# Performance work log

Hardware: AMD Instinct MI355X
Metric: run time of the kernel (lower is better)

Reference implementation:

```python
import jax, jax.numpy as jnp
import numpy as np

EPS = 1e-5
LORA_DIM = 64
LORA_SCALE = LORA_DIM ** (-0.5)
GRAD_SCALE = 0.5  # infeat_grad_scale (bp_to_unet=True path)


def _ln(x, g=None, b=None):
    mu = jnp.mean(x, axis=-1, keepdims=True)
    var = jnp.mean((x - mu) ** 2, axis=-1, keepdims=True)
    y = (x - mu) * jax.lax.rsqrt(var + EPS)
    if g is not None:
        y = y * g + b
    return y


def _grad_scale(t, s=GRAD_SCALE):
    # identity in forward, scales gradient by s in backward
    return t * s + jax.lax.stop_gradient(t) * (1.0 - s)


def setup_inputs() -> dict:
    key = jax.random.key(0)
    ks = jax.random.split(key, 8)
    B, C, H, W = 32, 1280, 32, 32
    TD, LD = 768, LORA_DIM
    inp = {}
    inp["layer_infeat"] = jax.random.normal(ks[0], (B, C, H, W), jnp.float32)
    inp["layer_inquery"] = jax.random.normal(ks[1], (B, H * W, C), jnp.float32)
    inp["token_q_emb"] = jax.random.normal(ks[2], (TD,), jnp.float32)
    # learned params
    inp["to_q_w"] = jax.random.normal(ks[3], (C, TD), jnp.float32) * (TD ** -0.5)
    inp["ln_x_g"] = jnp.ones((C,), jnp.float32)
    inp["ln_x_b"] = jnp.zeros((C,), jnp.float32)
    inp["ln_k_g"] = jnp.ones((C,), jnp.float32)
    inp["ln_k_b"] = jnp.zeros((C,), jnp.float32)
    inp["ln_q_g"] = jnp.ones((TD,), jnp.float32)
    inp["ln_q_b"] = jnp.zeros((TD,), jnp.float32)
    inp["lora_q_w"] = jax.random.normal(ks[4], (LD, C), jnp.float32) * (C ** -0.5)
    inp["lora_k_w"] = jax.random.normal(ks[5], (LD, C), jnp.float32) * (C ** -0.5)
    inp["mask"] = jax.random.randint(ks[6], (B, 1, H, W), 0, 2).astype(jnp.float32)
    return inp


def reference(layer_infeat, layer_inquery, token_q_emb, to_q_w,
              ln_x_g, ln_x_b, ln_k_g, ln_k_b, ln_q_g, ln_q_b,
              lora_q_w, lora_k_w, mask):
    B, C, H, W = layer_infeat.shape
    # flatten(2).permute(0,2,1): [B,C,H,W] -> [B, HW, C]
    x = _grad_scale(layer_infeat).reshape(B, C, H * W).transpose(0, 2, 1)
    k_in = _grad_scale(layer_inquery)
    # q = to_q(ln_q(token_q_emb[None])) -> [1, C], broadcast to [B, 1, C]
    q = _ln(token_q_emb[None, :], ln_q_g, ln_q_b) @ to_q_w.T
    q = jnp.broadcast_to(q[None], (B, 1, C))
    k = _ln(k_in, ln_k_g, ln_k_b)   # [B, HW, C]
    v = _ln(x, ln_x_g, ln_x_b)      # [B, HW, C]
    # LoRA score path (use_lora=True since lora_dim>0)
    lora_q = _ln(q) @ lora_q_w.T    # [B, 1, LD]
    lora_k = _ln(k) @ lora_k_w.T    # [B, HW, LD]
    sim = jnp.einsum('bid,bjd->bij', lora_q, lora_k) * LORA_SCALE  # [B,1,HW]
    # mask: nearest interpolation to (H,W) is identity (same size); flatten
    m = mask.reshape(B, 1, H * W) > 0
    sim = jnp.where(m, sim, -jnp.finfo(sim.dtype).max)
    attn = jax.nn.softmax(sim, axis=-1)
    fg = jnp.einsum('bij,bjd->bid', attn, v)            # [B, 1, C]
    bg = jnp.mean(v, axis=1, keepdims=True) - fg        # [B, 1, C]
    out = jnp.concatenate([fg, bg], axis=-1)            # [B, 1, 2C]
    return out[:, 0, :]                                  # [B, 2C]
```

## Files before the change

### kernel.cpp

```cpp
#include <hip/hip_runtime.h>
#include <math.h>

#define B_   32
#define CD   1280
#define HW_  1024
#define TD_  768
#define LD_  64
#define EPSF 1e-5f
#define LORA_SCALE_F 0.125f

__device__ __forceinline__ float wredSum(float a) {
#pragma unroll
  for (int o = 32; o; o >>= 1) a += __shfl_xor(a, o, 64);
  return a;
}
__device__ __forceinline__ void wred2(float& a, float& b) {
#pragma unroll
  for (int o = 32; o; o >>= 1) { a += __shfl_xor(a, o, 64); b += __shfl_xor(b, o, 64); }
}
__device__ __forceinline__ void wred3(float& a, float& b, float& c) {
#pragma unroll
  for (int o = 32; o; o >>= 1) {
    a += __shfl_xor(a, o, 64); b += __shfl_xor(b, o, 64); c += __shfl_xor(c, o, 64);
  }
}
template<int N>
__device__ __forceinline__ void wredN(float* v) {
#pragma unroll
  for (int o = 32; o; o >>= 1) {
#pragma unroll
    for (int k = 0; k < N; k++) v[k] += __shfl_xor(v[k], o, 64);
  }
}
__device__ __forceinline__ void blockSum2(float& a, float& b, float2* red) {
  int t = threadIdx.x;
  red[t] = make_float2(a, b); __syncthreads();
#pragma unroll
  for (int s = 128; s > 0; s >>= 1) {
    if (t < s) { red[t].x += red[t + s].x; red[t].y += red[t + s].y; }
    __syncthreads();
  }
  a = red[0].x; b = red[0].y; __syncthreads();
}

__global__ __launch_bounds__(256) void kA12(const float* __restrict__ tq,
                                            const float* __restrict__ lng,
                                            const float* __restrict__ lnb,
                                            const float* __restrict__ to_q_w,
                                            float* __restrict__ q_out) {
  __shared__ float lnq[TD_];
  __shared__ float2 red[256];
  int t = threadIdx.x;
  float s = 0.f, ss = 0.f, vals[3];
#pragma unroll
  for (int k = 0; k < 3; k++) { float v = tq[t + 256 * k]; vals[k] = v; s += v; ss += v * v; }
  blockSum2(s, ss, red);
  float mu = s * (1.f / TD_);
  float r = rsqrtf(ss * (1.f / TD_) - mu * mu + EPSF);
#pragma unroll
  for (int k = 0; k < 3; k++) { int i = t + 256 * k; lnq[i] = (vals[k] - mu) * r * lng[i] + lnb[i]; }
  __syncthreads();
  int c = blockIdx.x * 4 + (t >> 6);
  int lane = t & 63;
  const float4* w4 = (const float4*)(to_q_w + (size_t)c * TD_);
  const float4* l4 = (const float4*)lnq;
  float dot = 0.f;
#pragma unroll
  for (int i = 0; i < 3; i++) {
    int f = i * 64 + lane;
    float4 w = w4[f], l = l4[f];
    dot += w.x * l.x + w.y * l.y + w.z * l.z + w.w * l.w;
  }
  dot = wredSum(dot);
  if (lane == 0) q_out[c] = dot;
}

__global__ __launch_bounds__(256) void kA3456(const float* __restrict__ q_in,
                                              const float* __restrict__ lora_q_w,
                                              const float* __restrict__ lora_k_w,
                                              float* __restrict__ w_eff) {
  __shared__ float qn[CD];
  __shared__ float lq[LD_];
  __shared__ float redS[8];
  int t = threadIdx.x;
  int wid = t >> 6, lane = t & 63;
  float s = 0.f, ss = 0.f, vals[5];
#pragma unroll
  for (int k = 0; k < 5; k++) { float v = q_in[t + 256 * k]; vals[k] = v; s += v; ss += v * v; }
  wred2(s, ss);
  if (lane == 0) { redS[wid * 2] = s; redS[wid * 2 + 1] = ss; }
  __syncthreads();
  s = redS[0] + redS[2] + redS[4] + redS[6];
  ss = redS[1] + redS[3] + redS[5] + redS[7];
  float mu = s * (1.f / CD);
  float r = rsqrtf(ss * (1.f / CD) - mu * mu + EPSF);
#pragma unroll
  for (int k = 0; k < 5; k++) { int i = t + 256 * k; qn[i] = (vals[k] - mu) * r; }
  __syncthreads();
  {
    int gg = t >> 2, sub = t & 3;
    const float4* w4 = (const float4*)(lora_q_w + (size_t)gg * CD);
    const float4* q4 = (const float4*)qn;
    float dot = 0.f;
#pragma unroll 8
    for (int i = 0; i < 80; i++) {
      int f = i * 4 + sub;
      float4 w = w4[f], qq = q4[f];
      dot += w.x * qq.x + w.y * qq.y + w.z * qq.z + w.w * qq.w;
    }
    dot += __shfl_xor(dot, 1, 64);
    dot += __shfl_xor(dot, 2, 64);
    if (sub == 0) lq[gg] = dot;
  }
  __syncthreads();
  int c = blockIdx.x * 256 + t;
  float acc = 0.f;
#pragma unroll 8
  for (int d = 0; d < LD_; d++) acc += lq[d] * lora_k_w[(size_t)d * CD + c];
  w_eff[c] = acc;
}

__global__ __launch_bounds__(256, 4) void kBD1(const float* __restrict__ kin,
                                               const float* __restrict__ g,
                                               const float* __restrict__ bb,
                                               const float* __restrict__ w_eff,
                                               float* __restrict__ sim,
                                               const float* __restrict__ infeat,
                                               float* __restrict__ mu_out,
                                               float* __restrict__ r_out) {
  __shared__ float smem[5152];
  int t = threadIdx.x;
  int m5 = blockIdx.x % 5, d5 = blockIdx.x / 5;
  int wid = t >> 6, lane = t & 63;
  if (m5 != 4) {
    int kbid = d5 * 4 + m5;
    float* cg  = smem;
    float* cg2 = smem + 1280;
    float* cgb = smem + 2560;
    float* cwg = smem + 3840;
    float* red = smem + 5120;
    float p[8] = {0.f,0.f,0.f,0.f,0.f,0.f,0.f,0.f};
    for (int kk = t; kk < 320; kk += 256) {
      float4 g4 = ((const float4*)g)[kk];
      float4 b4 = ((const float4*)bb)[kk];
      float4 w4 = ((const float4*)w_eff)[kk];
      float4 q4  = make_float4(g4.x*g4.x, g4.y*g4.y, g4.z*g4.z, g4.w*g4.w);
      float4 gb4 = make_float4(g4.x*b4.x, g4.y*b4.y, g4.z*b4.z, g4.w*b4.w);
      float4 wg4 = make_float4(w4.x*g4.x, w4.y*g4.y, w4.z*g4.z, w4.w*g4.w);
      ((float4*)cg)[kk]  = g4;
      ((float4*)cg2)[kk] = q4;
      ((float4*)cgb)[kk] = gb4;
      ((float4*)cwg)[kk] = wg4;
      p[0] += g4.x + g4.y + g4.z + g4.w;
      p[1] += b4.x + b4.y + b4.z + b4.w;
      p[2] += q4.x + q4.y + q4.z + q4.w;
      p[3] += gb4.x + gb4.y + gb4.z + gb4.w;
      p[4] += b4.x*b4.x + b4.y*b4.y + b4.z*b4.z + b4.w*b4.w;
      p[5] += wg4.x + wg4.y + wg4.z + wg4.w;
      p[6] += w4.x*b4.x + w4.y*b4.y + w4.z*b4.z + w4.w*b4.w;
      p[7] += w4.x + w4.y + w4.z + w4.w;
    }
    wredN<8>(p);
    if (lane == 0) {
#pragma unroll
      for (int j = 0; j < 8; j++) red[wid * 8 + j] = p[j];
    }
    __syncthreads();
    float G0 = red[0] + red[8]  + red[16] + red[24];
    float B0 = red[1] + red[9]  + red[17] + red[25];
    float G2 = red[2] + red[10] + red[18] + red[26];
    float GB = red[3] + red[11] + red[19] + red[27];
    float B2 = red[4] + red[12] + red[20] + red[28];
    float WG = red[5] + red[13] + red[21] + red[29];
    float WB = red[6] + red[14] + red[22] + red[30];
    float W0 = red[7] + red[15] + red[23] + red[31];
    const float invC = 1.f / CD;
    const float4* cg4  = (const float4*)cg;
    const float4* cg24 = (const float4*)cg2;
    const float4* cgb4 = (const float4*)cgb;
    const float4* cwg4 = (const float4*)cwg;

    int gw = kbid * 4 + wid;
#pragma unroll
    for (int m = 0; m < 2; m++) {
      int rowA = gw + 16384 * m;
      int rowB = rowA + 8192;
      const float4* xA = (const float4*)(kin + (size_t)rowA * CD);
      const float4* xB = (const float4*)(kin + (size_t)rowB * CD);
      float v[14];
#pragma unroll
      for (int k = 0; k < 14; k++) v[k] = 0.f;
#pragma unroll
      for (int i = 0; i < 5; i++) {
        int f = i * 64 + lane;
        float4 xa = xA[f], xb = xB[f];
        float4 c1 = cg4[f], c2 = cg24[f], c3 = cgb4[f], c4 = cwg4[f];
#define ACC(X, Gc, G2c, GBc, WGc, o) { \
        float x_ = (X); float x2_ = x_ * x_; \
        v[(o)+0] += x_; v[(o)+1] += x2_; \
        v[(o)+2] = fmaf((Gc),  x_,  v[(o)+2]); \
        v[(o)+3] = fmaf((G2c), x_,  v[(o)+3]); \
        v[(o)+4] = fmaf((G2c), x2_, v[(o)+4]); \
        v[(o)+5] = fmaf((GBc), x_,  v[(o)+5]); \
        v[(o)+6] = fmaf((WGc), x_,  v[(o)+6]); }
        ACC(xa.x, c1.x, c2.x, c3.x, c4.x, 0)
        ACC(xa.y, c1.y, c2.y, c3.y, c4.y, 0)
        ACC(xa.z, c1.z, c2.z, c3.z, c4.z, 0)
        ACC(xa.w, c1.w, c2.w, c3.w, c4.w, 0)
        ACC(xb.x, c1.x, c2.x, c3.x, c4.x, 7)
        ACC(xb.y, c1.y, c2.y, c3.y, c4.y, 7)
        ACC(xb.z, c1.z, c2.z, c3.z, c4.z, 7)
        ACC(xb.w, c1.w, c2.w, c3.w, c4.w, 7)
#undef ACC
      }
      wredN<14>(v);
      float mu1a = v[0] * invC;
      float r1a  = rsqrtf(v[1] * invC - mu1a * mu1a + EPSF);
      float s2a  = r1a * (v[2] - mu1a * G0) + B0;
      float mu2a = s2a * invC;
      float ss2a = r1a * r1a * (v[4] - 2.f * mu1a * v[3] + mu1a * mu1a * G2)
                 + 2.f * r1a * (v[5] - mu1a * GB) + B2;
      float r2a  = rsqrtf(ss2a * invC - mu2a * mu2a + EPSF);
      float dta  = r1a * (v[6] - mu1a * WG) + WB;
      float simA = LORA_SCALE_F * r2a * (dta - mu2a * W0);
      float mu1b = v[7] * invC;
      float r1b  = rsqrtf(v[8] * invC - mu1b * mu1b + EPSF);
      float s2b  = r1b * (v[9] - mu1b * G0) + B0;
      float mu2b = s2b * invC;
      float ss2b = r1b * r1b * (v[11] - 2.f * mu1b * v[10] + mu1b * mu1b * G2)
                 + 2.f * r1b * (v[12] - mu1b * GB) + B2;
      float r2b  = rsqrtf(ss2b * invC - mu2b * mu2b + EPSF);
      float dtb  = r1b * (v[13] - mu1b * WG) + WB;
      float simB = LORA_SCALE_F * r2b * (dtb - mu2b * W0);
      if (lane == 0) { sim[rowA] = simA; sim[rowB] = simB; }
    }
  } else {
    int blk = d5;
    int tile = blk & 15, b = blk >> 4;
    int jg = t & 15;
    int slice = t >> 4;
    int j0 = tile * 64 + jg * 4;
    const float* base = infeat + (size_t)b * CD * HW_ + j0;
    float4 s = make_float4(0, 0, 0, 0), q = make_float4(0, 0, 0, 0);
    int c0 = slice * 80;
#pragma unroll 8
    for (int c = c0; c < c0 + 80; c++) {
      float4 v = *(const float4*)(base + (size_t)c * HW_);
      s.x += v.x; s.y += v.y; s.z += v.z; s.w += v.w;
      q.x += v.x * v.x; q.y += v.y * v.y; q.z += v.z * v.z; q.w += v.w * v.w;
    }
    float4* sArr = (float4*)smem;
    float4* qArr = ((float4*)smem) + 256;
    sArr[slice * 16 + jg] = s; qArr[slice * 16 + jg] = q;
    __syncthreads();
#pragma unroll
    for (int st = 8; st > 0; st >>= 1) {
      if (slice < st) {
        float4 a = sArr[slice * 16 + jg], b2 = sArr[(slice + st) * 16 + jg];
        a.x += b2.x; a.y += b2.y; a.z += b2.z; a.w += b2.w;
        sArr[slice * 16 + jg] = a;
        a = qArr[slice * 16 + jg]; b2 = qArr[(slice + st) * 16 + jg];
        a.x += b2.x; a.y += b2.y; a.z += b2.z; a.w += b2.w;
        qArr[slice * 16 + jg] = a;
      }
      __syncthreads();
    }
    if (slice == 0) {
      float4 S = sArr[jg], Q = qArr[jg], mu, r;
      mu.x = S.x * (1.f / CD); mu.y = S.y * (1.f / CD);
      mu.z = S.z * (1.f / CD); mu.w = S.w * (1.f / CD);
      r.x = rsqrtf(Q.x * (1.f / CD) - mu.x * mu.x + EPSF);
      r.y = rsqrtf(Q.y * (1.f / CD) - mu.y * mu.y + EPSF);
      r.z = rsqrtf(Q.z * (1.f / CD) - mu.z * mu.z + EPSF);
      r.w = rsqrtf(Q.w * (1.f / CD) - mu.w * mu.w + EPSF);
      int j = b * HW_ + j0;
      *(float4*)(mu_out + j) = mu;
      *(float4*)(r_out + j) = r;
    }
  }
}

__global__ __launch_bounds__(256, 4) void kD2f(const float* __restrict__ infeat,
                                               const float* __restrict__ sim,
                                               const float* __restrict__ mask,
                                               const float* __restrict__ mu,
                                               const float* __restrict__ r,
                                               const float* __restrict__ g,
                                               const float* __restrict__ bb,
                                               float* __restrict__ out) {
  __shared__ float4 w1s[HW_ / 4], w2s[HW_ / 4];
  __shared__ float red[16];
  int t = threadIdx.x;
  int b = blockIdx.x / 40, tile = blockIdx.x % 40;
  int wid = t >> 6, lane = t & 63;

  float4 sv = ((const float4*)(sim + b * HW_))[t];
  float4 mv = ((const float4*)(mask + b * HW_))[t];
  float4 muv = ((const float4*)(mu + b * HW_))[t];
  float4 rv = ((const float4*)(r + b * HW_))[t];
  const float NEG = -3.4028235e38f;
  float se0 = mv.x > 0.f ? sv.x : NEG;
  float se1 = mv.y > 0.f ? sv.y : NEG;
  float se2 = mv.z > 0.f ? sv.z : NEG;
  float se3 = mv.w > 0.f ? sv.w : NEG;
  float m = fmaxf(fmaxf(se0, se1), fmaxf(se2, se3));
#pragma unroll
  for (int o = 32; o; o >>= 1) m = fmaxf(m, __shfl_xor(m, o, 64));
  if (lane == 0) red[wid] = m;
  __syncthreads();
  float M = fmaxf(fmaxf(red[0], red[1]), fmaxf(red[2], red[3]));
  float e0 = expf(se0 - M), e1 = expf(se1 - M), e2 = expf(se2 - M), e3 = expf(se3 - M);
  float Z = e0 + e1 + e2 + e3;
  float t1 = e0 * rv.x * muv.x + e1 * rv.y * muv.y + e2 * rv.z * muv.z + e3 * rv.w * muv.w;
  float t3 = rv.x * muv.x + rv.y * muv.y + rv.z * muv.z + rv.w * muv.w;
  wred3(Z, t1, t3);
  __syncthreads();
  if (lane == 0) { red[4 + wid * 3] = Z; red[5 + wid * 3] = t1; red[6 + wid * 3] = t3; }
  __syncthreads();
  Z  = red[4] + red[7] + red[10] + red[13];
  t1 = red[5] + red[8] + red[11] + red[14];
  t3 = red[6] + red[9] + red[12] + red[15];
  float inv = 1.f / Z;
  float s1 = t1 * inv;
  float s3 = t3 * (1.f / HW_);
  w1s[t] = make_float4(e0 * rv.x * inv, e1 * rv.y * inv, e2 * rv.z * inv, e3 * rv.w * inv);
  w2s[t] = make_float4(rv.x * (1.f / HW_), rv.y * (1.f / HW_),
                       rv.z * (1.f / HW_), rv.w * (1.f / HW_));
  __syncthreads();

  int cbase = tile * 32 + wid * 8;
  const float* bbase = infeat + (size_t)b * CD * HW_;
  float v[16];
#pragma unroll
  for (int k = 0; k < 16; k++) v[k] = 0.f;
#pragma unroll
  for (int i = 0; i < 4; i++) {
    int f = i * 64 + lane;
    float4 a = w1s[f], w = w2s[f];
#pragma unroll
    for (int k = 0; k < 8; k++) {
      float4 x = ((const float4*)(bbase + (size_t)(cbase + k) * HW_))[f];
      v[2 * k]     += x.x * a.x + x.y * a.y + x.z * a.z + x.w * a.w;
      v[2 * k + 1] += x.x * w.x + x.y * w.y + x.z * w.z + x.w * w.w;
    }
  }
  wredN<16>(v);
  if (lane == 0) {
#pragma unroll
    for (int k = 0; k < 8; k++) {
      int c = cbase + k;
      float gc = g[c], bc = bb[c];
      float fg = gc * (v[2 * k] - s1) + bc;
      float vm = gc * (v[2 * k + 1] - s3) + bc;
      out[(size_t)b * (2 * CD) + c] = fg;
      out[(size_t)b * (2 * CD) + CD + c] = vm - fg;
    }
  }
}

extern "C" void kernel_launch(void* const* d_in, const int* in_sizes, int n_in,
                              void* d_out, int out_size, void* d_ws, size_t ws_size,
                              hipStream_t stream) {
  const float* infeat  = (const float*)d_in[0];
  const float* inquery = (const float*)d_in[1];
  const float* tq      = (const float*)d_in[2];
  const float* to_q_w  = (const float*)d_in[3];
  const float* ln_x_g  = (const float*)d_in[4];
  const float* ln_x_b  = (const float*)d_in[5];
  const float* ln_k_g  = (const float*)d_in[6];
  const float* ln_k_b  = (const float*)d_in[7];
  const float* ln_q_g  = (const float*)d_in[8];
  const float* ln_q_b  = (const float*)d_in[9];
  const float* lora_q_w = (const float*)d_in[10];
  const float* lora_k_w = (const float*)d_in[11];
  const float* mask    = (const float*)d_in[12];
  float* out = (float*)d_out;

  float* ws = (float*)d_ws;
  float* q_ws    = ws;
  float* weff_ws = ws + 1280;
  float* sim_ws  = ws + 2560;
  float* mu_ws   = ws + 35328;
  float* r_ws    = ws + 68096;

  kA12<<<320, 256, 0, stream>>>(tq, ln_q_g, ln_q_b, to_q_w, q_ws);
  kA3456<<<5, 256, 0, stream>>>(q_ws, lora_q_w, lora_k_w, weff_ws);
  kBD1<<<2560, 256, 0, stream>>>(inquery, ln_k_g, ln_k_b, weff_ws, sim_ws,
                                 infeat, mu_ws, r_ws);
  kD2f<<<1280, 256, 0, stream>>>(infeat, sim_ws, mask, mu_ws, r_ws,
                                 ln_x_g, ln_x_b, out);
}
```

Baseline: 416.0 us.

## Rebalance kBD1 block split, shrink shared memory, raise occupancy target

Changes the interleaving of LayerNorm-K blocks and infeat-stats blocks from 4:1 to 2:1, with smaller stats tiles (32 columns, 40-channel slices), and launches 3072 blocks. The shared-memory staging now holds g, b and w_eff instead of four precomputed products, and the accumulation uses u=g*x to form the same sums. Launch bounds rise to 8 blocks per CU. The goal is higher occupancy and better overlap of the two memory-bound streams, at the cost of a few extra multiplies per element and more register pressure under the tighter bound.

```diff
diff --git a/kernel.cpp b/kernel.cpp
--- a/kernel.cpp
+++ b/kernel.cpp
@@ -120,7 +120,7 @@
   w_eff[c] = acc;
 }
 
-__global__ __launch_bounds__(256, 4) void kBD1(const float* __restrict__ kin,
+__global__ __launch_bounds__(256, 8) void kBD1(const float* __restrict__ kin,
                                                const float* __restrict__ g,
                                                const float* __restrict__ bb,
                                                const float* __restrict__ w_eff,
@@ -128,35 +128,30 @@
                                                const float* __restrict__ infeat,
                                                float* __restrict__ mu_out,
                                                float* __restrict__ r_out) {
-  __shared__ float smem[5152];
-  int t = threadIdx.x;
-  int m5 = blockIdx.x % 5, d5 = blockIdx.x / 5;
+  __shared__ __align__(16) float smem[3872];
+  int t = threadIdx.x;
+  int m3 = blockIdx.x % 3, d3 = blockIdx.x / 3;
   int wid = t >> 6, lane = t & 63;
-  if (m5 != 4) {
-    int kbid = d5 * 4 + m5;
-    float* cg  = smem;
-    float* cg2 = smem + 1280;
-    float* cgb = smem + 2560;
-    float* cwg = smem + 3840;
-    float* red = smem + 5120;
+  if (m3 != 2) {
+    int kbid = d3 * 2 + m3;
+    float* cg = smem;
+    float* cb = smem + 1280;
+    float* cw = smem + 2560;
+    float* red = smem + 3840;
     float p[8] = {0.f,0.f,0.f,0.f,0.f,0.f,0.f,0.f};
     for (int kk = t; kk < 320; kk += 256) {
       float4 g4 = ((const float4*)g)[kk];
       float4 b4 = ((const float4*)bb)[kk];
       float4 w4 = ((const float4*)w_eff)[kk];
-      float4 q4  = make_float4(g4.x*g4.x, g4.y*g4.y, g4.z*g4.z, g4.w*g4.w);
-      float4 gb4 = make_float4(g4.x*b4.x, g4.y*b4.y, g4.z*b4.z, g4.w*b4.w);
-      float4 wg4 = make_float4(w4.x*g4.x, w4.y*g4.y, w4.z*g4.z, w4.w*g4.w);
-      ((float4*)cg)[kk]  = g4;
-      ((float4*)cg2)[kk] = q4;
-      ((float4*)cgb)[kk] = gb4;
-      ((float4*)cwg)[kk] = wg4;
+      ((float4*)cg)[kk] = g4;
+      ((float4*)cb)[kk] = b4;
+      ((float4*)cw)[kk] = w4;
       p[0] += g4.x + g4.y + g4.z + g4.w;
       p[1] += b4.x + b4.y + b4.z + b4.w;
-      p[2] += q4.x + q4.y + q4.z + q4.w;
-      p[3] += gb4.x + gb4.y + gb4.z + gb4.w;
+      p[2] += g4.x*g4.x + g4.y*g4.y + g4.z*g4.z + g4.w*g4.w;
+      p[3] += g4.x*b4.x + g4.y*b4.y + g4.z*b4.z + g4.w*b4.w;
       p[4] += b4.x*b4.x + b4.y*b4.y + b4.z*b4.z + b4.w*b4.w;
-      p[5] += wg4.x + wg4.y + wg4.z + wg4.w;
+      p[5] += w4.x*g4.x + w4.y*g4.y + w4.z*g4.z + w4.w*g4.w;
       p[6] += w4.x*b4.x + w4.y*b4.y + w4.z*b4.z + w4.w*b4.w;
       p[7] += w4.x + w4.y + w4.z + w4.w;
     }
@@ -175,10 +170,9 @@
     float WB = red[6] + red[14] + red[22] + red[30];
     float W0 = red[7] + red[15] + red[23] + red[31];
     const float invC = 1.f / CD;
-    const float4* cg4  = (const float4*)cg;
-    const float4* cg24 = (const float4*)cg2;
-    const float4* cgb4 = (const float4*)cgb;
-    const float4* cwg4 = (const float4*)cwg;
+    const float4* cg4 = (const float4*)cg;
+    const float4* cb4 = (const float4*)cb;
+    const float4* cw4 = (const float4*)cw;
 
     int gw = kbid * 4 + wid;
 #pragma unroll
@@ -194,23 +188,24 @@
       for (int i = 0; i < 5; i++) {
         int f = i * 64 + lane;
         float4 xa = xA[f], xb = xB[f];
-        float4 c1 = cg4[f], c2 = cg24[f], c3 = cgb4[f], c4 = cwg4[f];
-#define ACC(X, Gc, G2c, GBc, WGc, o) { \
-        float x_ = (X); float x2_ = x_ * x_; \
-        v[(o)+0] += x_; v[(o)+1] += x2_; \
-        v[(o)+2] = fmaf((Gc),  x_,  v[(o)+2]); \
-        v[(o)+3] = fmaf((G2c), x_,  v[(o)+3]); \
-        v[(o)+4] = fmaf((G2c), x2_, v[(o)+4]); \
-        v[(o)+5] = fmaf((GBc), x_,  v[(o)+5]); \
-        v[(o)+6] = fmaf((WGc), x_,  v[(o)+6]); }
-        ACC(xa.x, c1.x, c2.x, c3.x, c4.x, 0)
-        ACC(xa.y, c1.y, c2.y, c3.y, c4.y, 0)
-        ACC(xa.z, c1.z, c2.z, c3.z, c4.z, 0)
-        ACC(xa.w, c1.w, c2.w, c3.w, c4.w, 0)
-        ACC(xb.x, c1.x, c2.x, c3.x, c4.x, 7)
-        ACC(xb.y, c1.y, c2.y, c3.y, c4.y, 7)
-        ACC(xb.z, c1.z, c2.z, c3.z, c4.z, 7)
-        ACC(xb.w, c1.w, c2.w, c3.w, c4.w, 7)
+        float4 gc = cg4[f], bc = cb4[f], wc = cw4[f];
+#define ACC(X, Gc, Bc, Wc, o) { \
+        float x_ = (X); float u_ = (Gc) * x_; \
+        v[(o)+0] += x_; \
+        v[(o)+1] = fmaf(x_, x_, v[(o)+1]); \
+        v[(o)+2] += u_; \
+        v[(o)+3] = fmaf(u_, u_, v[(o)+3]); \
+        v[(o)+4] = fmaf((Gc), u_, v[(o)+4]); \
+        v[(o)+5] = fmaf((Bc), u_, v[(o)+5]); \
+        v[(o)+6] = fmaf((Wc), u_, v[(o)+6]); }
+        ACC(xa.x, gc.x, bc.x, wc.x, 0)
+        ACC(xa.y, gc.y, bc.y, wc.y, 0)
+        ACC(xa.z, gc.z, bc.z, wc.z, 0)
+        ACC(xa.w, gc.w, bc.w, wc.w, 0)
+        ACC(xb.x, gc.x, bc.x, wc.x, 7)
+        ACC(xb.y, gc.y, bc.y, wc.y, 7)
+        ACC(xb.z, gc.z, bc.z, wc.z, 7)
+        ACC(xb.w, gc.w, bc.w, wc.w, 7)
 #undef ACC
       }
       wredN<14>(v);
@@ -218,7 +213,7 @@
       float r1a  = rsqrtf(v[1] * invC - mu1a * mu1a + EPSF);
       float s2a  = r1a * (v[2] - mu1a * G0) + B0;
       float mu2a = s2a * invC;
-      float ss2a = r1a * r1a * (v[4] - 2.f * mu1a * v[3] + mu1a * mu1a * G2)
+      float ss2a = r1a * r1a * (v[3] - 2.f * mu1a * v[4] + mu1a * mu1a * G2)
                  + 2.f * r1a * (v[5] - mu1a * GB) + B2;
       float r2a  = rsqrtf(ss2a * invC - mu2a * mu2a + EPSF);
       float dta  = r1a * (v[6] - mu1a * WG) + WB;
@@ -227,7 +222,7 @@
       float r1b  = rsqrtf(v[8] * invC - mu1b * mu1b + EPSF);
       float s2b  = r1b * (v[9] - mu1b * G0) + B0;
       float mu2b = s2b * invC;
-      float ss2b = r1b * r1b * (v[11] - 2.f * mu1b * v[10] + mu1b * mu1b * G2)
+      float ss2b = r1b * r1b * (v[10] - 2.f * mu1b * v[11] + mu1b * mu1b * G2)
                  + 2.f * r1b * (v[12] - mu1b * GB) + B2;
       float r2b  = rsqrtf(ss2b * invC - mu2b * mu2b + EPSF);
       float dtb  = r1b * (v[13] - mu1b * WG) + WB;
@@ -235,33 +230,33 @@
       if (lane == 0) { sim[rowA] = simA; sim[rowB] = simB; }
     }
   } else {
-    int blk = d5;
-    int tile = blk & 15, b = blk >> 4;
-    int jg = t & 15;
-    int slice = t >> 4;
-    int j0 = tile * 64 + jg * 4;
+    int blk = d3;
+    int b = blk >> 5, tile = blk & 31;
+    int jg = t & 7;
+    int slice = t >> 3;
+    int j0 = tile * 32 + jg * 4;
     const float* base = infeat + (size_t)b * CD * HW_ + j0;
     float4 s = make_float4(0, 0, 0, 0), q = make_float4(0, 0, 0, 0);
-    int c0 = slice * 80;
+    int c0 = slice * 40;
 #pragma unroll 8
-    for (int c = c0; c < c0 + 80; c++) {
+    for (int c = c0; c < c0 + 40; c++) {
       float4 v = *(const float4*)(base + (size_t)c * HW_);
       s.x += v.x; s.y += v.y; s.z += v.z; s.w += v.w;
       q.x += v.x * v.x; q.y += v.y * v.y; q.z += v.z * v.z; q.w += v.w * v.w;
     }
     float4* sArr = (float4*)smem;
     float4* qArr = ((float4*)smem) + 256;
-    sArr[slice * 16 + jg] = s; qArr[slice * 16 + jg] = q;
+    sArr[slice * 8 + jg] = s; qArr[slice * 8 + jg] = q;
     __syncthreads();
 #pragma unroll
-    for (int st = 8; st > 0; st >>= 1) {
+    for (int st = 16; st > 0; st >>= 1) {
       if (slice < st) {
-        float4 a = sArr[slice * 16 + jg], b2 = sArr[(slice + st) * 16 + jg];
+        float4 a = sArr[slice * 8 + jg], b2 = sArr[(slice + st) * 8 + jg];
         a.x += b2.x; a.y += b2.y; a.z += b2.z; a.w += b2.w;
-        sArr[slice * 16 + jg] = a;
-        a = qArr[slice * 16 + jg]; b2 = qArr[(slice + st) * 16 + jg];
+        sArr[slice * 8 + jg] = a;
+        a = qArr[slice * 8 + jg]; b2 = qArr[(slice + st) * 8 + jg];
         a.x += b2.x; a.y += b2.y; a.z += b2.z; a.w += b2.w;
-        qArr[slice * 16 + jg] = a;
+        qArr[slice * 8 + jg] = a;
       }
       __syncthreads();
     }
@@ -385,7 +380,7 @@
 
   kA12<<<320, 256, 0, stream>>>(tq, ln_q_g, ln_q_b, to_q_w, q_ws);
   kA3456<<<5, 256, 0, stream>>>(q_ws, lora_q_w, lora_k_w, weff_ws);
-  kBD1<<<2560, 256, 0, stream>>>(inquery, ln_k_g, ln_k_b, weff_ws, sim_ws,
+  kBD1<<<3072, 256, 0, stream>>>(inquery, ln_k_g, ln_k_b, weff_ws, sim_ws,
                                  infeat, mu_ws, r_ws);
   kD2f<<<1280, 256, 0, stream>>>(infeat, sim_ws, mask, mu_ws, r_ws,
                                  ln_x_g, ln_x_b, out);
```

Measured after the change: 451.0 us. 8.4% more time.
